# Performance work log

Hardware: AMD Instinct MI355X
Metric: run time of the kernel (lower is better)

## Reference

```python
import jax, jax.numpy as jnp
import numpy as np

N_HEADS = 12
HEAD_DIM = 64
EMB_DIM = 768
ATTN_DIM = N_HEADS * HEAD_DIM


def setup_inputs() -> dict:
    key = jax.random.key(0)
    k1, k2, k3, k4 = jax.random.split(key, 4)
    B, N = 8, 1024
    x = jax.random.normal(k1, (B, N, EMB_DIM), dtype=jnp.float32)
    scale = 1.0 / np.sqrt(EMB_DIM)
    w_qkv = jax.random.normal(k2, (EMB_DIM, 3 * ATTN_DIM), dtype=jnp.float32) * scale
    w_out = jax.random.normal(k3, (ATTN_DIM, EMB_DIM), dtype=jnp.float32) * (1.0 / np.sqrt(ATTN_DIM))
    b_out = jax.random.normal(k4, (EMB_DIM,), dtype=jnp.float32) * 0.01
    return {"x": x, "w_qkv": w_qkv, "w_out": w_out, "b_out": b_out}


def reference(x, w_qkv, w_out, b_out):
    B, N, _ = x.shape
    qkv = jnp.einsum('bnd,de->bne', x, w_qkv)  # [B,N,3*attn_dim]
    q, k, v = jnp.split(qkv, 3, axis=-1)
    # [B, n_heads, N, head_dim]
    def heads(t):
        return t.reshape(B, N, N_HEADS, HEAD_DIM).transpose(0, 2, 1, 3)
    q, k, v = heads(q), heads(k), heads(v)
    scores = jnp.einsum('bhnd,bhmd->bhnm', q, k) * (HEAD_DIM ** -0.5)
    attn = jax.nn.softmax(scores, axis=-1)
    out = jnp.einsum('bhnm,bhmd->bhnd', attn, v)
    out = out.transpose(0, 2, 1, 3).reshape(B, N, ATTN_DIM)
    return jnp.einsum('bnd,de->bne', out, w_out) + b_out
```

## Files before the change

### kernel.cpp

```cpp
#include <hip/hip_runtime.h>
#include <hip/hip_bf16.h>

typedef unsigned short u16;
typedef __attribute__((ext_vector_type(8))) short short8;
typedef __attribute__((ext_vector_type(4))) float floatx4;

#define SEQ    1024
#define EMB    768
#define NHEADS 12
#define HDIM   64
#define QKVD   2304
#define BATCH  8
#define ROWS   8192
#define QKW    1536

__device__ __forceinline__ u16 f2bf(float f) {
  unsigned int x; __builtin_memcpy(&x, &f, 4);
  x = (x + 0x7FFFu + ((x >> 16) & 1u)) >> 16;
  return (u16)x;
}
__device__ __forceinline__ unsigned int pack2bf_t(float a, float b) {
  unsigned int ua, ub;
  __builtin_memcpy(&ua, &a, 4); __builtin_memcpy(&ub, &b, 4);
  return (ub & 0xFFFF0000u) | (ua >> 16);
}

__device__ __forceinline__ void gld16(const void* g, void* l) {
  __builtin_amdgcn_global_load_lds(
      (const __attribute__((address_space(1))) void*)g,
      (__attribute__((address_space(3))) void*)l, 16, 0, 0);
}

__global__ __launch_bounds__(256) void f2bf_vec(const float* __restrict__ src,
                                                u16* __restrict__ dst, int n) {
  const int i = (blockIdx.x * 256 + threadIdx.x) * 8;
  if (i >= n) return;
  u16 tmp[8];
#pragma unroll
  for (int j = 0; j < 8; ++j) tmp[j] = f2bf(src[i + j]);
  *(uint4*)(dst + i) = *(const uint4*)tmp;
}

__global__ __launch_bounds__(256) void transpose_f2bf(const float* __restrict__ in,
                                                      u16* __restrict__ out,
                                                      int R, int C) {
  __shared__ u16 tile[32][33];
  const int c0 = blockIdx.x * 32, r0 = blockIdx.y * 32;
  const int tx = threadIdx.x, ty = threadIdx.y;
#pragma unroll
  for (int i = 0; i < 4; ++i)
    tile[ty + i * 8][tx] = f2bf(in[(size_t)(r0 + ty + i * 8) * C + c0 + tx]);
  __syncthreads();
#pragma unroll
  for (int i = 0; i < 4; ++i)
    out[(size_t)(c0 + ty + i * 8) * R + r0 + tx] = tile[tx][ty + i * 8];
}

__global__ __launch_bounds__(256) void gemm_qkv(const u16* __restrict__ A,
                                                const u16* __restrict__ Bt,
                                                u16* __restrict__ qk,
                                                u16* __restrict__ vT) {
  constexpr int K = EMB;
  __shared__ __align__(16) u16 As[128 * 64];
  __shared__ __align__(16) u16 Bs[128 * 64];
  const int t = threadIdx.x;
  const int w = t >> 6, lane = t & 63, l16 = lane & 15, quad = lane >> 4;
  const int wm = (w >> 1) * 64, wn = (w & 1) * 64;
  const int flat = blockIdx.y * 18 + blockIdx.x;
  const int grp = flat / 144, loc = flat % 144;
  const int m0 = (grp * 8 + (loc & 7)) * 128;
  const int n0 = (loc >> 3) * 128;

  floatx4 acc[4][4];
#pragma unroll
  for (int mt = 0; mt < 4; ++mt)
#pragma unroll
    for (int nt = 0; nt < 4; ++nt) acc[mt][nt] = (floatx4){0.f, 0.f, 0.f, 0.f};

  for (int k0 = 0; k0 < K; k0 += 64) {
    __syncthreads();
#pragma unroll
    for (int i = 0; i < 4; ++i) {
      const int idx = i * 256 + t;
      const int row = idx >> 3;
      const int gc8 = (((idx & 7) ^ (row & 7)) << 3);
      gld16(A  + (size_t)(m0 + row) * K + k0 + gc8, As + (size_t)idx * 8);
      gld16(Bt + (size_t)(n0 + row) * K + k0 + gc8, Bs + (size_t)idx * 8);
    }
    __syncthreads();

#pragma unroll
    for (int kk = 0; kk < 2; ++kk) {
      short8 a[4], b[4];
#pragma unroll
      for (int mt = 0; mt < 4; ++mt) {
        const int row = wm + mt * 16 + l16;
        a[mt] = *(const short8*)(As + row * 64 + ((((kk << 2) + quad) ^ (row & 7)) << 3));
      }
#pragma unroll
      for (int nt = 0; nt < 4; ++nt) {
        const int row = wn + nt * 16 + l16;
        b[nt] = *(const short8*)(Bs + row * 64 + ((((kk << 2) + quad) ^ (row & 7)) << 3));
      }
#pragma unroll
      for (int mt = 0; mt < 4; ++mt)
#pragma unroll
        for (int nt = 0; nt < 4; ++nt)
          acc[mt][nt] = __builtin_amdgcn_mfma_f32_16x16x32_bf16(a[mt], b[nt], acc[mt][nt], 0, 0, 0);
    }
  }

  if (n0 < QKW) {
#pragma unroll
    for (int mt = 0; mt < 4; ++mt)
#pragma unroll
      for (int nt = 0; nt < 4; ++nt) {
        const int col = n0 + wn + nt * 16 + l16;
#pragma unroll
        for (int r = 0; r < 4; ++r) {
          const int row = m0 + wm + mt * 16 + quad * 4 + r;
          qk[(size_t)row * QKW + col] = f2bf(acc[mt][nt][r]);
        }
      }
  } else {
#pragma unroll
    for (int mt = 0; mt < 4; ++mt) {
      const int rowb = m0 + wm + mt * 16 + quad * 4;
      const int b = rowb >> 10, n = rowb & 1023;
#pragma unroll
      for (int nt = 0; nt < 4; ++nt) {
        const int vc = n0 + wn + nt * 16 + l16 - QKW;
        const int h = vc >> 6, d = vc & 63;
        ushort4 pk;
        pk.x = f2bf(acc[mt][nt][0]); pk.y = f2bf(acc[mt][nt][1]);
        pk.z = f2bf(acc[mt][nt][2]); pk.w = f2bf(acc[mt][nt][3]);
        *(ushort4*)(vT + ((size_t)(b * NHEADS + h) * HDIM + d) * SEQ + n) = pk;
      }
    }
  }
}

__global__ __launch_bounds__(256) void flash_attn(const u16* __restrict__ qk,
                                                  const u16* __restrict__ vT,
                                                  u16* __restrict__ aout) {
  __shared__ __align__(16) u16 QPs[128 * 64];
  __shared__ __align__(16) u16 Ks[64 * 64];
  __shared__ __align__(16) u16 Vs[64 * 64];

  const int t = threadIdx.x;
  const int w = t >> 6, lane = t & 63, l16 = lane & 15, quad = lane >> 4;
  const int bh = blockIdx.x, b = bh / NHEADS, h = bh % NHEADS;
  const int m0 = blockIdx.y * 128;
  constexpr float C_EXP = 0.125f * 1.44269504f;

  const size_t qbase = (size_t)(b * SEQ + m0) * QKW + h * HDIM;
#pragma unroll
  for (int i = 0; i < 4; ++i) {
    const int idx = i * 256 + t, row = idx >> 3, c = idx & 7;
    *(uint4*)(QPs + row * 64 + ((c ^ (row & 7)) << 3)) =
        *(const uint4*)(qk + qbase + (size_t)row * QKW + (c << 3));
  }
  __syncthreads();

  short8 bq[2][2];
#pragma unroll
  for (int mt = 0; mt < 2; ++mt)
#pragma unroll
    for (int kc = 0; kc < 2; ++kc)
      bq[mt][kc] = *(const short8*)(QPs + (w * 32 + mt * 16 + l16) * 64 +
                                    ((((kc << 2) + quad) ^ (l16 & 7)) << 3));

  float l_r[2] = {0.f, 0.f};
  floatx4 o[2][4];
#pragma unroll
  for (int mt = 0; mt < 2; ++mt)
#pragma unroll
    for (int ct = 0; ct < 4; ++ct) o[mt][ct] = (floatx4){0.f, 0.f, 0.f, 0.f};

  const size_t kbase = (size_t)(b * SEQ) * QKW + EMB + h * HDIM;
  const size_t vbase = (size_t)bh * HDIM * SEQ;
  u16* Pw = QPs + w * 32 * 64;

  for (int n0 = 0; n0 < SEQ; n0 += 64) {
    __syncthreads();
#pragma unroll
    for (int i = 0; i < 2; ++i) {
      const int idx = i * 256 + t, kr = idx >> 3;
      const int gc = (((idx & 7) ^ (kr & 7)) << 3);
      gld16(qk + kbase + (size_t)(n0 + kr) * QKW + gc, Ks + (size_t)idx * 8);
      gld16(vT + vbase + (size_t)kr * SEQ + n0 + gc,   Vs + (size_t)idx * 8);
    }
    __syncthreads();

    floatx4 st[4][2];
#pragma unroll
    for (int kt = 0; kt < 4; ++kt)
#pragma unroll
      for (int mt = 0; mt < 2; ++mt) st[kt][mt] = (floatx4){0.f, 0.f, 0.f, 0.f};
#pragma unroll
    for (int kt = 0; kt < 4; ++kt) {
      const int krow = (kt * 16 + l16) * 64;
      const short8 ak0 = *(const short8*)(Ks + krow + (((0 + quad) ^ (l16 & 7)) << 3));
      const short8 ak1 = *(const short8*)(Ks + krow + (((4 + quad) ^ (l16 & 7)) << 3));
#pragma unroll
      for (int mt = 0; mt < 2; ++mt) {
        st[kt][mt] = __builtin_amdgcn_mfma_f32_16x16x32_bf16(ak0, bq[mt][0], st[kt][mt], 0, 0, 0);
        st[kt][mt] = __builtin_amdgcn_mfma_f32_16x16x32_bf16(ak1, bq[mt][1], st[kt][mt], 0, 0, 0);
      }
    }

#pragma unroll
    for (int mt = 0; mt < 2; ++mt) {
      float lacc = 0.f;
#pragma unroll
      for (int kt = 0; kt < 4; ++kt) {
        const float p0 = __builtin_amdgcn_exp2f(st[kt][mt][0] * C_EXP);
        const float p1 = __builtin_amdgcn_exp2f(st[kt][mt][1] * C_EXP);
        const float p2 = __builtin_amdgcn_exp2f(st[kt][mt][2] * C_EXP);
        const float p3 = __builtin_amdgcn_exp2f(st[kt][mt][3] * C_EXP);
        lacc += (p0 + p1) + (p2 + p3);
        uint2 pw2;
        pw2.x = pack2bf_t(p0, p1);
        pw2.y = pack2bf_t(p2, p3);
        *(uint2*)(Pw + (mt * 16 + l16) * 64 +
                  ((((kt << 1) + (quad >> 1)) ^ (l16 & 7)) << 3) + (quad & 1) * 4) = pw2;
      }
      l_r[mt] += lacc;
    }

#pragma unroll
    for (int kk = 0; kk < 2; ++kk) {
      const int sl = (((kk << 2) + quad) ^ (l16 & 7)) << 3;
      const short8 ap0 = *(const short8*)(Pw + (0 * 16 + l16) * 64 + sl);
      const short8 ap1 = *(const short8*)(Pw + (1 * 16 + l16) * 64 + sl);
#pragma unroll
      for (int ct = 0; ct < 4; ++ct) {
        const short8 bv = *(const short8*)(Vs + (ct * 16 + l16) * 64 + sl);
        o[0][ct] = __builtin_amdgcn_mfma_f32_16x16x32_bf16(ap0, bv, o[0][ct], 0, 0, 0);
        o[1][ct] = __builtin_amdgcn_mfma_f32_16x16x32_bf16(ap1, bv, o[1][ct], 0, 0, 0);
      }
    }
  }

  float invs[2][4];
#pragma unroll
  for (int mt = 0; mt < 2; ++mt) {
    float l = l_r[mt];
    l += __shfl_xor(l, 16);
    l += __shfl_xor(l, 32);
    const float iv = 1.f / l;
#pragma unroll
    for (int r = 0; r < 4; ++r) invs[mt][r] = __shfl(iv, quad * 4 + r);
  }
#pragma unroll
  for (int mt = 0; mt < 2; ++mt)
#pragma unroll
    for (int ct = 0; ct < 4; ++ct)
#pragma unroll
      for (int r = 0; r < 4; ++r) {
        const int row = m0 + w * 32 + mt * 16 + quad * 4 + r;
        const int col = h * HDIM + ct * 16 + l16;
        aout[(size_t)(b * SEQ + row) * EMB + col] = f2bf(o[mt][ct][r] * invs[mt][r]);
      }
}

__global__ __launch_bounds__(256) void gemm_out(const u16* __restrict__ A,
                                                const u16* __restrict__ Bt,
                                                const float* __restrict__ bias,
                                                float* __restrict__ C) {
  constexpr int K = EMB, N = EMB;
  __shared__ __align__(16) u16 As[64 * 64];
  __shared__ __align__(16) u16 Bs[128 * 64];
  const int t = threadIdx.x;
  const int w = t >> 6, lane = t & 63, l16 = lane & 15, quad = lane >> 4;
  const int wm = (w >> 1) * 32, wn = (w & 1) * 64;
  const int flat = blockIdx.y * 6 + blockIdx.x;
  const int grp = flat / 48, loc = flat % 48;
  const int m0 = (grp * 8 + (loc & 7)) * 64;
  const int n0 = (loc >> 3) * 128;

  floatx4 acc[2][4];
#pragma unroll
  for (int mt = 0; mt < 2; ++mt)
#pragma unroll
    for (int nt = 0; nt < 4; ++nt) acc[mt][nt] = (floatx4){0.f, 0.f, 0.f, 0.f};

  for (int k0 = 0; k0 < K; k0 += 64) {
    __syncthreads();
#pragma unroll
    for (int i = 0; i < 2; ++i) {
      const int idx = i * 256 + t;
      const int row = idx >> 3;
      const int gc8 = (((idx & 7) ^ (row & 7)) << 3);
      gld16(A + (size_t)(m0 + row) * K + k0 + gc8, As + (size_t)idx * 8);
    }
#pragma unroll
    for (int i = 0; i < 4; ++i) {
      const int idx = i * 256 + t;
      const int row = idx >> 3;
      const int gc8 = (((idx & 7) ^ (row & 7)) << 3);
      gld16(Bt + (size_t)(n0 + row) * K + k0 + gc8, Bs + (size_t)idx * 8);
    }
    __syncthreads();

#pragma unroll
    for (int kk = 0; kk < 2; ++kk) {
      short8 a[2], b[4];
#pragma unroll
      for (int mt = 0; mt < 2; ++mt) {
        const int row = wm + mt * 16 + l16;
        a[mt] = *(const short8*)(As + row * 64 + ((((kk << 2) + quad) ^ (row & 7)) << 3));
      }
#pragma unroll
      for (int nt = 0; nt < 4; ++nt) {
        const int row = wn + nt * 16 + l16;
        b[nt] = *(const short8*)(Bs + row * 64 + ((((kk << 2) + quad) ^ (row & 7)) << 3));
      }
#pragma unroll
      for (int mt = 0; mt < 2; ++mt)
#pragma unroll
        for (int nt = 0; nt < 4; ++nt)
          acc[mt][nt] = __builtin_amdgcn_mfma_f32_16x16x32_bf16(a[mt], b[nt], acc[mt][nt], 0, 0, 0);
    }
  }

#pragma unroll
  for (int mt = 0; mt < 2; ++mt)
#pragma unroll
    for (int nt = 0; nt < 4; ++nt) {
      const int col = n0 + wn + nt * 16 + l16;
      const float badd = bias[col];
#pragma unroll
      for (int r = 0; r < 4; ++r) {
        const int row = m0 + wm + mt * 16 + quad * 4 + r;
        C[(size_t)row * N + col] = acc[mt][nt][r] + badd;
      }
    }
}

extern "C" void kernel_launch(void* const* d_in, const int* in_sizes, int n_in,
                              void* d_out, int out_size, void* d_ws, size_t ws_size,
                              hipStream_t stream) {
  const float* x     = (const float*)d_in[0];
  const float* w_qkv = (const float*)d_in[1];
  const float* w_out = (const float*)d_in[2];
  const float* b_out = (const float*)d_in[3];
  float* out = (float*)d_out;

  u16* qk    = (u16*)d_ws;
  u16* vT    = qk    + (size_t)ROWS * QKW;
  u16* xb    = vT    + (size_t)BATCH * NHEADS * HDIM * SEQ;
  u16* aout  = xb;
  u16* wqkvT = xb    + (size_t)ROWS * EMB;
  u16* woutT = wqkvT + (size_t)QKVD * EMB;

  f2bf_vec<<<ROWS * EMB / 8 / 256, 256, 0, stream>>>(x, xb, ROWS * EMB);
  transpose_f2bf<<<dim3(QKVD / 32, EMB / 32), dim3(32, 8), 0, stream>>>(w_qkv, wqkvT, EMB, QKVD);
  transpose_f2bf<<<dim3(EMB / 32, EMB / 32), dim3(32, 8), 0, stream>>>(w_out, woutT, EMB, EMB);

  gemm_qkv<<<dim3(18, 64), 256, 0, stream>>>(xb, wqkvT, qk, vT);

  flash_attn<<<dim3(BATCH * NHEADS, SEQ / 128), 256, 0, stream>>>(qk, vT, aout);

  gemm_out<<<dim3(6, 128), 256, 0, stream>>>(aout, woutT, b_out, out);
}
```

Measured before the change: 194.8 us.

## Double-buffer LDS tiles in GEMMs and attention; merge weight transposes into one launch

Adds two-stage LDS double buffering to gemm_qkv, flash_attn and gemm_out. The next K/V or A/B tile is issued through global_load_lds before the current tile is computed, and explicit vmcnt waits plus s_barrier replace the paired __syncthreads, so global load latency can overlap MFMA work. The two weight transpose launches are also folded into one kernel launch. LDS use doubles per block, which may lower occupancy, and the hand-written vmcnt counts must match the number of loads issued per stage.

```diff
diff --git a/kernel.cpp b/kernel.cpp
--- a/kernel.cpp
+++ b/kernel.cpp
@@ -31,6 +31,9 @@
       (__attribute__((address_space(3))) void*)l, 16, 0, 0);
 }
 
+#define PIPE_BARRIER_VM(N) asm volatile("s_waitcnt vmcnt(" #N ")\n\ts_barrier" ::: "memory")
+#define PIPE_BARRIER       asm volatile("s_barrier" ::: "memory")
+
 __global__ __launch_bounds__(256) void f2bf_vec(const float* __restrict__ src,
                                                 u16* __restrict__ dst, int n) {
   const int i = (blockIdx.x * 256 + threadIdx.x) * 8;
@@ -41,11 +44,17 @@
   *(uint4*)(dst + i) = *(const uint4*)tmp;
 }
 
-__global__ __launch_bounds__(256) void transpose_f2bf(const float* __restrict__ in,
-                                                      u16* __restrict__ out,
-                                                      int R, int C) {
+__global__ __launch_bounds__(256) void transpose_w(const float* __restrict__ wqkv,
+                                                   const float* __restrict__ wout,
+                                                   u16* __restrict__ dqkv,
+                                                   u16* __restrict__ dout) {
   __shared__ u16 tile[32][33];
-  const int c0 = blockIdx.x * 32, r0 = blockIdx.y * 32;
+  const bool second = blockIdx.x >= 72;
+  const float* in = second ? wout : wqkv;
+  u16* out = second ? dout : dqkv;
+  const int C = second ? EMB : QKVD;
+  const int bx = second ? blockIdx.x - 72 : blockIdx.x;
+  const int c0 = bx * 32, r0 = blockIdx.y * 32;
   const int tx = threadIdx.x, ty = threadIdx.y;
 #pragma unroll
   for (int i = 0; i < 4; ++i)
@@ -53,16 +62,16 @@
   __syncthreads();
 #pragma unroll
   for (int i = 0; i < 4; ++i)
-    out[(size_t)(c0 + ty + i * 8) * R + r0 + tx] = tile[tx][ty + i * 8];
+    out[(size_t)(c0 + ty + i * 8) * EMB + r0 + tx] = tile[tx][ty + i * 8];
 }
 
 __global__ __launch_bounds__(256) void gemm_qkv(const u16* __restrict__ A,
                                                 const u16* __restrict__ Bt,
                                                 u16* __restrict__ qk,
                                                 u16* __restrict__ vT) {
-  constexpr int K = EMB;
-  __shared__ __align__(16) u16 As[128 * 64];
-  __shared__ __align__(16) u16 Bs[128 * 64];
+  constexpr int K = EMB, ITERS = K / 64;
+  __shared__ __align__(16) u16 As[2][128 * 64];
+  __shared__ __align__(16) u16 Bs[2][128 * 64];
   const int t = threadIdx.x;
   const int w = t >> 6, lane = t & 63, l16 = lane & 15, quad = lane >> 4;
   const int wm = (w >> 1) * 64, wn = (w & 1) * 64;
@@ -71,36 +80,44 @@
   const int m0 = (grp * 8 + (loc & 7)) * 128;
   const int n0 = (loc >> 3) * 128;
 
-  floatx4 acc[4][4];
-#pragma unroll
-  for (int mt = 0; mt < 4; ++mt)
-#pragma unroll
-    for (int nt = 0; nt < 4; ++nt) acc[mt][nt] = (floatx4){0.f, 0.f, 0.f, 0.f};
-
-  for (int k0 = 0; k0 < K; k0 += 64) {
-    __syncthreads();
+  auto stage = [&](int k0, int buf) {
 #pragma unroll
     for (int i = 0; i < 4; ++i) {
       const int idx = i * 256 + t;
       const int row = idx >> 3;
       const int gc8 = (((idx & 7) ^ (row & 7)) << 3);
-      gld16(A  + (size_t)(m0 + row) * K + k0 + gc8, As + (size_t)idx * 8);
-      gld16(Bt + (size_t)(n0 + row) * K + k0 + gc8, Bs + (size_t)idx * 8);
-    }
-    __syncthreads();
-
+      gld16(A  + (size_t)(m0 + row) * K + k0 + gc8, &As[buf][(size_t)idx * 8]);
+      gld16(Bt + (size_t)(n0 + row) * K + k0 + gc8, &Bs[buf][(size_t)idx * 8]);
+    }
+  };
+
+  floatx4 acc[4][4];
+#pragma unroll
+  for (int mt = 0; mt < 4; ++mt)
+#pragma unroll
+    for (int nt = 0; nt < 4; ++nt) acc[mt][nt] = (floatx4){0.f, 0.f, 0.f, 0.f};
+
+  stage(0, 0);
+  for (int it = 0; it < ITERS; ++it) {
+    const int cur = it & 1;
+    if (it + 1 < ITERS) {
+      stage((it + 1) * 64, cur ^ 1);
+      PIPE_BARRIER_VM(8);
+    } else {
+      PIPE_BARRIER_VM(0);
+    }
 #pragma unroll
     for (int kk = 0; kk < 2; ++kk) {
       short8 a[4], b[4];
 #pragma unroll
       for (int mt = 0; mt < 4; ++mt) {
         const int row = wm + mt * 16 + l16;
-        a[mt] = *(const short8*)(As + row * 64 + ((((kk << 2) + quad) ^ (row & 7)) << 3));
+        a[mt] = *(const short8*)(&As[cur][row * 64 + ((((kk << 2) + quad) ^ (row & 7)) << 3)]);
       }
 #pragma unroll
       for (int nt = 0; nt < 4; ++nt) {
         const int row = wn + nt * 16 + l16;
-        b[nt] = *(const short8*)(Bs + row * 64 + ((((kk << 2) + quad) ^ (row & 7)) << 3));
+        b[nt] = *(const short8*)(&Bs[cur][row * 64 + ((((kk << 2) + quad) ^ (row & 7)) << 3)]);
       }
 #pragma unroll
       for (int mt = 0; mt < 4; ++mt)
@@ -108,6 +125,7 @@
         for (int nt = 0; nt < 4; ++nt)
           acc[mt][nt] = __builtin_amdgcn_mfma_f32_16x16x32_bf16(a[mt], b[nt], acc[mt][nt], 0, 0, 0);
     }
+    PIPE_BARRIER;
   }
 
   if (n0 < QKW) {
@@ -144,14 +162,30 @@
                                                   const u16* __restrict__ vT,
                                                   u16* __restrict__ aout) {
   __shared__ __align__(16) u16 QPs[128 * 64];
-  __shared__ __align__(16) u16 Ks[64 * 64];
-  __shared__ __align__(16) u16 Vs[64 * 64];
+  __shared__ __align__(16) u16 Ks[2][64 * 64];
+  __shared__ __align__(16) u16 Vs[2][64 * 64];
 
   const int t = threadIdx.x;
   const int w = t >> 6, lane = t & 63, l16 = lane & 15, quad = lane >> 4;
   const int bh = blockIdx.x, b = bh / NHEADS, h = bh % NHEADS;
   const int m0 = blockIdx.y * 128;
   constexpr float C_EXP = 0.125f * 1.44269504f;
+  constexpr int ITERS = SEQ / 64;
+
+  const size_t kbase = (size_t)(b * SEQ) * QKW + EMB + h * HDIM;
+  const size_t vbase = (size_t)bh * HDIM * SEQ;
+
+  auto stage = [&](int n0, int buf) {
+#pragma unroll
+    for (int i = 0; i < 2; ++i) {
+      const int idx = i * 256 + t, kr = idx >> 3;
+      const int gc = (((idx & 7) ^ (kr & 7)) << 3);
+      gld16(qk + kbase + (size_t)(n0 + kr) * QKW + gc, &Ks[buf][(size_t)idx * 8]);
+      gld16(vT + vbase + (size_t)kr * SEQ + n0 + gc,   &Vs[buf][(size_t)idx * 8]);
+    }
+  };
+
+  stage(0, 0);
 
   const size_t qbase = (size_t)(b * SEQ + m0) * QKW + h * HDIM;
 #pragma unroll
@@ -177,20 +211,16 @@
 #pragma unroll
     for (int ct = 0; ct < 4; ++ct) o[mt][ct] = (floatx4){0.f, 0.f, 0.f, 0.f};
 
-  const size_t kbase = (size_t)(b * SEQ) * QKW + EMB + h * HDIM;
-  const size_t vbase = (size_t)bh * HDIM * SEQ;
   u16* Pw = QPs + w * 32 * 64;
 
-  for (int n0 = 0; n0 < SEQ; n0 += 64) {
-    __syncthreads();
-#pragma unroll
-    for (int i = 0; i < 2; ++i) {
-      const int idx = i * 256 + t, kr = idx >> 3;
-      const int gc = (((idx & 7) ^ (kr & 7)) << 3);
-      gld16(qk + kbase + (size_t)(n0 + kr) * QKW + gc, Ks + (size_t)idx * 8);
-      gld16(vT + vbase + (size_t)kr * SEQ + n0 + gc,   Vs + (size_t)idx * 8);
-    }
-    __syncthreads();
+  for (int it = 0; it < ITERS; ++it) {
+    const int cur = it & 1;
+    if (it + 1 < ITERS) {
+      stage((it + 1) * 64, cur ^ 1);
+      PIPE_BARRIER_VM(4);
+    } else {
+      PIPE_BARRIER_VM(0);
+    }
 
     floatx4 st[4][2];
 #pragma unroll
@@ -200,8 +230,8 @@
 #pragma unroll
     for (int kt = 0; kt < 4; ++kt) {
       const int krow = (kt * 16 + l16) * 64;
-      const short8 ak0 = *(const short8*)(Ks + krow + (((0 + quad) ^ (l16 & 7)) << 3));
-      const short8 ak1 = *(const short8*)(Ks + krow + (((4 + quad) ^ (l16 & 7)) << 3));
+      const short8 ak0 = *(const short8*)(&Ks[cur][krow + (((0 + quad) ^ (l16 & 7)) << 3)]);
+      const short8 ak1 = *(const short8*)(&Ks[cur][krow + (((4 + quad) ^ (l16 & 7)) << 3)]);
 #pragma unroll
       for (int mt = 0; mt < 2; ++mt) {
         st[kt][mt] = __builtin_amdgcn_mfma_f32_16x16x32_bf16(ak0, bq[mt][0], st[kt][mt], 0, 0, 0);
@@ -235,11 +265,12 @@
       const short8 ap1 = *(const short8*)(Pw + (1 * 16 + l16) * 64 + sl);
 #pragma unroll
       for (int ct = 0; ct < 4; ++ct) {
-        const short8 bv = *(const short8*)(Vs + (ct * 16 + l16) * 64 + sl);
+        const short8 bv = *(const short8*)(&Vs[cur][(ct * 16 + l16) * 64 + sl]);
         o[0][ct] = __builtin_amdgcn_mfma_f32_16x16x32_bf16(ap0, bv, o[0][ct], 0, 0, 0);
         o[1][ct] = __builtin_amdgcn_mfma_f32_16x16x32_bf16(ap1, bv, o[1][ct], 0, 0, 0);
       }
     }
+    PIPE_BARRIER;
   }
 
   float invs[2][4];
@@ -268,9 +299,9 @@
                                                 const u16* __restrict__ Bt,
                                                 const float* __restrict__ bias,
                                                 float* __restrict__ C) {
-  constexpr int K = EMB, N = EMB;
-  __shared__ __align__(16) u16 As[64 * 64];
-  __shared__ __align__(16) u16 Bs[128 * 64];
+  constexpr int K = EMB, N = EMB, ITERS = K / 64;
+  __shared__ __align__(16) u16 As[2][64 * 64];
+  __shared__ __align__(16) u16 Bs[2][128 * 64];
   const int t = threadIdx.x;
   const int w = t >> 6, lane = t & 63, l16 = lane & 15, quad = lane >> 4;
   const int wm = (w >> 1) * 32, wn = (w & 1) * 64;
@@ -279,42 +310,50 @@
   const int m0 = (grp * 8 + (loc & 7)) * 64;
   const int n0 = (loc >> 3) * 128;
 
-  floatx4 acc[2][4];
-#pragma unroll
-  for (int mt = 0; mt < 2; ++mt)
-#pragma unroll
-    for (int nt = 0; nt < 4; ++nt) acc[mt][nt] = (floatx4){0.f, 0.f, 0.f, 0.f};
-
-  for (int k0 = 0; k0 < K; k0 += 64) {
-    __syncthreads();
+  auto stage = [&](int k0, int buf) {
 #pragma unroll
     for (int i = 0; i < 2; ++i) {
       const int idx = i * 256 + t;
       const int row = idx >> 3;
       const int gc8 = (((idx & 7) ^ (row & 7)) << 3);
-      gld16(A + (size_t)(m0 + row) * K + k0 + gc8, As + (size_t)idx * 8);
+      gld16(A + (size_t)(m0 + row) * K + k0 + gc8, &As[buf][(size_t)idx * 8]);
     }
 #pragma unroll
     for (int i = 0; i < 4; ++i) {
       const int idx = i * 256 + t;
       const int row = idx >> 3;
       const int gc8 = (((idx & 7) ^ (row & 7)) << 3);
-      gld16(Bt + (size_t)(n0 + row) * K + k0 + gc8, Bs + (size_t)idx * 8);
-    }
-    __syncthreads();
-
+      gld16(Bt + (size_t)(n0 + row) * K + k0 + gc8, &Bs[buf][(size_t)idx * 8]);
+    }
+  };
+
+  floatx4 acc[2][4];
+#pragma unroll
+  for (int mt = 0; mt < 2; ++mt)
+#pragma unroll
+    for (int nt = 0; nt < 4; ++nt) acc[mt][nt] = (floatx4){0.f, 0.f, 0.f, 0.f};
+
+  stage(0, 0);
+  for (int it = 0; it < ITERS; ++it) {
+    const int cur = it & 1;
+    if (it + 1 < ITERS) {
+      stage((it + 1) * 64, cur ^ 1);
+      PIPE_BARRIER_VM(6);
+    } else {
+      PIPE_BARRIER_VM(0);
+    }
 #pragma unroll
     for (int kk = 0; kk < 2; ++kk) {
       short8 a[2], b[4];
 #pragma unroll
       for (int mt = 0; mt < 2; ++mt) {
         const int row = wm + mt * 16 + l16;
-        a[mt] = *(const short8*)(As + row * 64 + ((((kk << 2) + quad) ^ (row & 7)) << 3));
+        a[mt] = *(const short8*)(&As[cur][row * 64 + ((((kk << 2) + quad) ^ (row & 7)) << 3)]);
       }
 #pragma unroll
       for (int nt = 0; nt < 4; ++nt) {
         const int row = wn + nt * 16 + l16;
-        b[nt] = *(const short8*)(Bs + row * 64 + ((((kk << 2) + quad) ^ (row & 7)) << 3));
+        b[nt] = *(const short8*)(&Bs[cur][row * 64 + ((((kk << 2) + quad) ^ (row & 7)) << 3)]);
       }
 #pragma unroll
       for (int mt = 0; mt < 2; ++mt)
@@ -322,6 +361,7 @@
         for (int nt = 0; nt < 4; ++nt)
           acc[mt][nt] = __builtin_amdgcn_mfma_f32_16x16x32_bf16(a[mt], b[nt], acc[mt][nt], 0, 0, 0);
     }
+    PIPE_BARRIER;
   }
 
 #pragma unroll
@@ -355,8 +395,7 @@
   u16* woutT = wqkvT + (size_t)QKVD * EMB;
 
   f2bf_vec<<<ROWS * EMB / 8 / 256, 256, 0, stream>>>(x, xb, ROWS * EMB);
-  transpose_f2bf<<<dim3(QKVD / 32, EMB / 32), dim3(32, 8), 0, stream>>>(w_qkv, wqkvT, EMB, QKVD);
-  transpose_f2bf<<<dim3(EMB / 32, EMB / 32), dim3(32, 8), 0, stream>>>(w_out, woutT, EMB, EMB);
+  transpose_w<<<dim3(96, 24), dim3(32, 8), 0, stream>>>(w_qkv, w_out, wqkvT, woutT);
 
   gemm_qkv<<<dim3(18, 64), 256, 0, stream>>>(xb, wqkvT, qk, vT);
 
```

Result: faster. 179.9 us (-7.6%).
